# Optimization experiments

Measured on AMD Instinct MI355X. Metric: run time of the kernel, lower is better.

The kernel has to match this reference:

```python
import jax, jax.numpy as jnp
import numpy as np

N_SAMPLES = 8388608  # total packed samples across all rays
N_RAYS = 131072      # number of rays (segments)


def setup_inputs() -> dict:
    key = jax.random.key(0)
    k1, k2, k3 = jax.random.split(key, 3)
    # Sorted segment ids emulate the packed ray layout (samples of a ray are contiguous).
    segment_ids = jnp.sort(
        jax.random.randint(k1, (N_SAMPLES,), 0, N_RAYS, dtype=jnp.int32)
    )
    rgb_samples = jax.random.normal(k2, (N_SAMPLES, 3), dtype=jnp.float32)
    weights_samples = jax.random.uniform(k3, (N_SAMPLES, 1), dtype=jnp.float32)
    return {
        "segment_ids": segment_ids,
        "rgb_samples": rgb_samples,
        "weights_samples": weights_samples,
        "n_rays": N_RAYS,
    }


def reference(segment_ids, rgb_samples, weights_samples, n_rays):
    # pred_rgb[r] = sum over samples s belonging to ray r of w_s * rgb_s
    weighted = rgb_samples * weights_samples  # [N,3], weight broadcast over channels
    pred_rgb = jax.ops.segment_sum(weighted, segment_ids, num_segments=n_rays)  # [n_rays,3]
    return pred_rgb
```

## Files before the change

kernel.cpp:

```cpp
#include <hip/hip_runtime.h>


#define NTHREADS 256

__global__ __launch_bounds__(NTHREADS) void zero_out_kernel(float4* __restrict__ out4,
                                                            int n4) {
  int i = blockIdx.x * blockDim.x + threadIdx.x;
  if (i < n4) out4[i] = make_float4(0.f, 0.f, 0.f, 0.f);
}

__global__ __launch_bounds__(NTHREADS) void integrate_kernel(
    const int* __restrict__ ids, const float* __restrict__ rgb,
    const float* __restrict__ w, float* __restrict__ out, int n_samples) {
  const int lane = threadIdx.x & 63;
  const long long t0 = (long long)(blockIdx.x * blockDim.x + threadIdx.x) * 4;

  int idv[4];
  float px[4], py[4], pz[4];
  if (t0 + 3 < n_samples) {
    const int4   id4 = *(const int4*)(ids + t0);
    const float4 w4  = *(const float4*)(w + t0);
    const float4 r0  = *(const float4*)(rgb + 3 * t0);
    const float4 r1  = *(const float4*)(rgb + 3 * t0 + 4);
    const float4 r2  = *(const float4*)(rgb + 3 * t0 + 8);
    idv[0] = id4.x; idv[1] = id4.y; idv[2] = id4.z; idv[3] = id4.w;
    px[0] = r0.x * w4.x; py[0] = r0.y * w4.x; pz[0] = r0.z * w4.x;
    px[1] = r0.w * w4.y; py[1] = r1.x * w4.y; pz[1] = r1.y * w4.y;
    px[2] = r1.z * w4.z; py[2] = r1.w * w4.z; pz[2] = r2.x * w4.z;
    px[3] = r2.y * w4.w; py[3] = r2.z * w4.w; pz[3] = r2.w * w4.w;
  } else {
    int last = ids[n_samples - 1];
    #pragma unroll
    for (int j = 0; j < 4; ++j) {
      long long s = t0 + j;
      if (s < n_samples) {
        idv[j] = ids[s];
        float ww = w[s];
        px[j] = rgb[3 * s + 0] * ww;
        py[j] = rgb[3 * s + 1] * ww;
        pz[j] = rgb[3 * s + 2] * ww;
      } else {
        idv[j] = (j == 0) ? last : idv[j - 1];
        px[j] = py[j] = pz[j] = 0.f;
      }
    }
  }

  const int id0 = idv[0], id3 = idv[3];
  const bool f_intra = (id0 != id3);
  const int hl = (idv[1] == id0) ? ((idv[2] == id0) ? ((idv[3] == id0) ? 4 : 3) : 2) : 1;
  const int tl = (idv[2] == id3) ? ((idv[1] == id3) ? ((idv[0] == id3) ? 4 : 3) : 2) : 1;
  float hx = 0.f, hy = 0.f, hz = 0.f, tx = 0.f, ty = 0.f, tz = 0.f;
  #pragma unroll
  for (int j = 0; j < 4; ++j) {
    if (j < hl)     { hx += px[j]; hy += py[j]; hz += pz[j]; }
    if (j >= 4 - tl){ tx += px[j]; ty += py[j]; tz += pz[j]; }
  }
  {
    int ilo = hl, ihi = 3 - tl;
    if (ilo <= ihi) {
      if (ilo == ihi) {
        atomicAdd(&out[3 * idv[ilo] + 0], px[ilo]);
        atomicAdd(&out[3 * idv[ilo] + 1], py[ilo]);
        atomicAdd(&out[3 * idv[ilo] + 2], pz[ilo]);
      } else if (idv[ilo] == idv[ihi]) {
        atomicAdd(&out[3 * idv[ilo] + 0], px[ilo] + px[ihi]);
        atomicAdd(&out[3 * idv[ilo] + 1], py[ilo] + py[ihi]);
        atomicAdd(&out[3 * idv[ilo] + 2], pz[ilo] + pz[ihi]);
      } else {
        atomicAdd(&out[3 * idv[ilo] + 0], px[ilo]);
        atomicAdd(&out[3 * idv[ilo] + 1], py[ilo]);
        atomicAdd(&out[3 * idv[ilo] + 2], pz[ilo]);
        atomicAdd(&out[3 * idv[ihi] + 0], px[ihi]);
        atomicAdd(&out[3 * idv[ihi] + 1], py[ihi]);
        atomicAdd(&out[3 * idv[ihi] + 2], pz[ihi]);
      }
    }
  }

  const int prev_tid = __shfl_up(id3, 1, 64);
  int fl = (lane == 0 || f_intra || prev_tid != id0) ? 1 : 0;
  float sx = tx, sy = ty, sz = tz;
  #pragma unroll
  for (int off = 1; off < 64; off <<= 1) {
    float ox = __shfl_up(sx, off, 64);
    float oy = __shfl_up(sy, off, 64);
    float oz = __shfl_up(sz, off, 64);
    int  ofl = __shfl_up(fl, off, 64);
    if (lane >= off && fl == 0) { sx += ox; sy += oy; sz += oz; fl = ofl; }
  }

  const float pSx = __shfl_up(sx, 1, 64);
  const float pSy = __shfl_up(sy, 1, 64);
  const float pSz = __shfl_up(sz, 1, 64);
  if (f_intra) {
    const bool link = (lane > 0) && (prev_tid == id0);
    atomicAdd(&out[3 * id0 + 0], hx + (link ? pSx : 0.f));
    atomicAdd(&out[3 * id0 + 1], hy + (link ? pSy : 0.f));
    atomicAdd(&out[3 * id0 + 2], hz + (link ? pSz : 0.f));
  }

  const int next_hid = __shfl_down(id0, 1, 64);
  if (lane == 63 || next_hid != id3) {
    atomicAdd(&out[3 * id3 + 0], sx);
    atomicAdd(&out[3 * id3 + 1], sy);
    atomicAdd(&out[3 * id3 + 2], sz);
  }
}

extern "C" void kernel_launch(void* const* d_in, const int* in_sizes, int n_in,
                              void* d_out, int out_size, void* d_ws, size_t ws_size,
                              hipStream_t stream) {
  const int*   segment_ids = (const int*)d_in[0];
  const float* rgb         = (const float*)d_in[1];
  const float* weights     = (const float*)d_in[2];
  float*       out         = (float*)d_out;

  const int n_samples = in_sizes[0];

  {
    int n4 = out_size / 4;
    int blocks = (n4 + NTHREADS - 1) / NTHREADS;
    zero_out_kernel<<<blocks, NTHREADS, 0, stream>>>((float4*)out, n4);
  }
  {
    int spb = NTHREADS * 4;
    int blocks = (n_samples + spb - 1) / spb;
    integrate_kernel<<<blocks, NTHREADS, 0, stream>>>(
        segment_ids, rgb, weights, out, n_samples);
  }
}
```

Baseline: 194.6 us.

## Use persistent waves with software-prefetched chunks and ballot-based segmented scan

The integrate kernel becomes a grid-stride persistent kernel capped at 1024 blocks. Each wave loads its next 256-sample chunk before processing the current one, so memory latency overlaps with the scan and atomics. The segmented scan now finds each lane's segment start once with a ballot and count-leading-zeros, which removes the per-step flag shuffle. This raises register pressure because two chunks are live at once, and fewer blocks may lower occupancy for this bandwidth-bound streaming load.

```diff
diff --git a/kernel.cpp b/kernel.cpp
--- a/kernel.cpp
+++ b/kernel.cpp
@@ -2,6 +2,8 @@
 
 
 #define NTHREADS 256
+#define WPB      (NTHREADS / 64)
+#define NBLOCKS  1024
 
 __global__ __launch_bounds__(NTHREADS) void zero_out_kernel(float4* __restrict__ out4,
                                                             int n4) {
@@ -9,42 +11,59 @@
   if (i < n4) out4[i] = make_float4(0.f, 0.f, 0.f, 0.f);
 }
 
-__global__ __launch_bounds__(NTHREADS) void integrate_kernel(
-    const int* __restrict__ ids, const float* __restrict__ rgb,
-    const float* __restrict__ w, float* __restrict__ out, int n_samples) {
-  const int lane = threadIdx.x & 63;
-  const long long t0 = (long long)(blockIdx.x * blockDim.x + threadIdx.x) * 4;
+struct Chunk {
+  int4 id4;
+  float4 w4, r0, r1, r2;
+};
 
-  int idv[4];
-  float px[4], py[4], pz[4];
+__device__ __forceinline__ Chunk load_chunk(const int* __restrict__ ids,
+                                            const float* __restrict__ rgb,
+                                            const float* __restrict__ w,
+                                            long long t0, int n_samples) {
+  Chunk c;
   if (t0 + 3 < n_samples) {
-    const int4   id4 = *(const int4*)(ids + t0);
-    const float4 w4  = *(const float4*)(w + t0);
-    const float4 r0  = *(const float4*)(rgb + 3 * t0);
-    const float4 r1  = *(const float4*)(rgb + 3 * t0 + 4);
-    const float4 r2  = *(const float4*)(rgb + 3 * t0 + 8);
-    idv[0] = id4.x; idv[1] = id4.y; idv[2] = id4.z; idv[3] = id4.w;
-    px[0] = r0.x * w4.x; py[0] = r0.y * w4.x; pz[0] = r0.z * w4.x;
-    px[1] = r0.w * w4.y; py[1] = r1.x * w4.y; pz[1] = r1.y * w4.y;
-    px[2] = r1.z * w4.z; py[2] = r1.w * w4.z; pz[2] = r2.x * w4.z;
-    px[3] = r2.y * w4.w; py[3] = r2.z * w4.w; pz[3] = r2.w * w4.w;
+    c.id4 = *(const int4*)(ids + t0);
+    c.w4  = *(const float4*)(w + t0);
+    c.r0  = *(const float4*)(rgb + 3 * t0);
+    c.r1  = *(const float4*)(rgb + 3 * t0 + 4);
+    c.r2  = *(const float4*)(rgb + 3 * t0 + 8);
   } else {
-    int last = ids[n_samples - 1];
+    int lastid = ids[n_samples - 1];
+    int   it[4];
+    float wt[4], rt[12];
     #pragma unroll
     for (int j = 0; j < 4; ++j) {
       long long s = t0 + j;
       if (s < n_samples) {
-        idv[j] = ids[s];
-        float ww = w[s];
-        px[j] = rgb[3 * s + 0] * ww;
-        py[j] = rgb[3 * s + 1] * ww;
-        pz[j] = rgb[3 * s + 2] * ww;
+        it[j] = ids[s];
+        wt[j] = w[s];
+        rt[3 * j + 0] = rgb[3 * s + 0];
+        rt[3 * j + 1] = rgb[3 * s + 1];
+        rt[3 * j + 2] = rgb[3 * s + 2];
       } else {
-        idv[j] = (j == 0) ? last : idv[j - 1];
-        px[j] = py[j] = pz[j] = 0.f;
+        it[j] = lastid;
+        wt[j] = 0.f;
+        rt[3 * j + 0] = rt[3 * j + 1] = rt[3 * j + 2] = 0.f;
       }
     }
+    c.id4 = make_int4(it[0], it[1], it[2], it[3]);
+    c.w4  = make_float4(wt[0], wt[1], wt[2], wt[3]);
+    c.r0  = make_float4(rt[0], rt[1], rt[2], rt[3]);
+    c.r1  = make_float4(rt[4], rt[5], rt[6], rt[7]);
+    c.r2  = make_float4(rt[8], rt[9], rt[10], rt[11]);
   }
+  return c;
+}
+
+__device__ __forceinline__ void process_chunk(const Chunk& c,
+                                              float* __restrict__ out,
+                                              int lane) {
+  const int idv[4] = {c.id4.x, c.id4.y, c.id4.z, c.id4.w};
+  float px[4], py[4], pz[4];
+  px[0] = c.r0.x * c.w4.x; py[0] = c.r0.y * c.w4.x; pz[0] = c.r0.z * c.w4.x;
+  px[1] = c.r0.w * c.w4.y; py[1] = c.r1.x * c.w4.y; pz[1] = c.r1.y * c.w4.y;
+  px[2] = c.r1.z * c.w4.z; py[2] = c.r1.w * c.w4.z; pz[2] = c.r2.x * c.w4.z;
+  px[3] = c.r2.y * c.w4.w; py[3] = c.r2.z * c.w4.w; pz[3] = c.r2.w * c.w4.w;
 
   const int id0 = idv[0], id3 = idv[3];
   const bool f_intra = (id0 != id3);
@@ -53,8 +72,8 @@
   float hx = 0.f, hy = 0.f, hz = 0.f, tx = 0.f, ty = 0.f, tz = 0.f;
   #pragma unroll
   for (int j = 0; j < 4; ++j) {
-    if (j < hl)     { hx += px[j]; hy += py[j]; hz += pz[j]; }
-    if (j >= 4 - tl){ tx += px[j]; ty += py[j]; tz += pz[j]; }
+    if (j < hl)      { hx += px[j]; hy += py[j]; hz += pz[j]; }
+    if (j >= 4 - tl) { tx += px[j]; ty += py[j]; tz += pz[j]; }
   }
   {
     int ilo = hl, ihi = 3 - tl;
@@ -79,15 +98,17 @@
   }
 
   const int prev_tid = __shfl_up(id3, 1, 64);
-  int fl = (lane == 0 || f_intra || prev_tid != id0) ? 1 : 0;
+  const int fl = (lane == 0 || f_intra || prev_tid != id0) ? 1 : 0;
+  const unsigned long long heads = __ballot(fl);
+  const unsigned long long below = heads & (~0ull >> (63 - lane));
+  const int start = 63 - __clzll(below);
   float sx = tx, sy = ty, sz = tz;
   #pragma unroll
   for (int off = 1; off < 64; off <<= 1) {
     float ox = __shfl_up(sx, off, 64);
     float oy = __shfl_up(sy, off, 64);
     float oz = __shfl_up(sz, off, 64);
-    int  ofl = __shfl_up(fl, off, 64);
-    if (lane >= off && fl == 0) { sx += ox; sy += oy; sz += oz; fl = ofl; }
+    if (lane - off >= start) { sx += ox; sy += oy; sz += oz; }
   }
 
   const float pSx = __shfl_up(sx, 1, 64);
@@ -108,6 +129,30 @@
   }
 }
 
+__global__ __launch_bounds__(NTHREADS) void integrate_kernel(
+    const int* __restrict__ ids, const float* __restrict__ rgb,
+    const float* __restrict__ w, float* __restrict__ out, int n_samples) {
+  const int lane = threadIdx.x & 63;
+  const int wave = blockIdx.x * WPB + (threadIdx.x >> 6);
+  const int W    = gridDim.x * WPB;
+  const int nchunks = (n_samples + 255) >> 8;
+
+  int c = wave;
+  if (c >= nchunks) return;
+  Chunk cur = load_chunk(ids, rgb, w, (long long)c * 256 + lane * 4, n_samples);
+  for (;;) {
+    const int cn = c + W;
+    const bool has_next = (cn < nchunks);
+    Chunk nxt;
+    if (has_next)
+      nxt = load_chunk(ids, rgb, w, (long long)cn * 256 + lane * 4, n_samples);
+    process_chunk(cur, out, lane);
+    if (!has_next) break;
+    cur = nxt;
+    c = cn;
+  }
+}
+
 extern "C" void kernel_launch(void* const* d_in, const int* in_sizes, int n_in,
                               void* d_out, int out_size, void* d_ws, size_t ws_size,
                               hipStream_t stream) {
@@ -124,8 +169,9 @@
     zero_out_kernel<<<blocks, NTHREADS, 0, stream>>>((float4*)out, n4);
   }
   {
-    int spb = NTHREADS * 4;
-    int blocks = (n_samples + spb - 1) / spb;
+    int nchunks = (n_samples + 255) / 256;
+    int blocks_needed = (nchunks + WPB - 1) / WPB;
+    int blocks = blocks_needed < NBLOCKS ? blocks_needed : NBLOCKS;
     integrate_kernel<<<blocks, NTHREADS, 0, stream>>>(
         segment_ids, rgb, weights, out, n_samples);
   }
```

Result: slower. 200.7 us (+3.2%).
